# Kernel tuning notes

Hardware: AMD Instinct MI355X
Metric: run time of the kernel (lower is better)

The kernel has to match this reference:

```python
import jax, jax.numpy as jnp
import numpy as np

EPS = 1e-6

def _conv1x1(x, w, bias):
    # x: [b,cin,h,w], w: [cout,cin]
    y = jnp.einsum('bchw,oc->bohw', x, w)
    return y + bias[None, :, None, None]

def _maxpool2(x):
    b, c, h, w = x.shape
    return x.reshape(b, c, h // 2, 2, w // 2, 2).max(axis=(3, 5))

def _up2_align_corners(x):
    # bilinear upsample x2, align_corners=True (matches torch nn.Upsample)
    b, c, h, w = x.shape
    oh, ow = 2 * h, 2 * w
    ys = jnp.linspace(0.0, h - 1.0, oh)
    xs = jnp.linspace(0.0, w - 1.0, ow)
    y0 = jnp.floor(ys).astype(jnp.int32); y1 = jnp.minimum(y0 + 1, h - 1)
    x0 = jnp.floor(xs).astype(jnp.int32); x1 = jnp.minimum(x0 + 1, w - 1)
    ty = (ys - y0).reshape(1, 1, oh, 1)
    tx = (xs - x0).reshape(1, 1, 1, ow)
    r0 = x[:, :, y0, :]; r1 = x[:, :, y1, :]           # [b,c,oh,w]
    v00 = r0[:, :, :, x0]; v01 = r0[:, :, :, x1]       # [b,c,oh,ow]
    v10 = r1[:, :, :, x0]; v11 = r1[:, :, :, x1]
    return (1 - ty) * ((1 - tx) * v00 + tx * v01) + ty * ((1 - tx) * v10 + tx * v11)

def _norm_corr(fm):
    # fm: [b,N,N], indexed [b,p,q]; ReLU then L2-normalize over q for each p
    m = jnp.maximum(fm, 0.0)
    norm = jnp.sqrt(jnp.sum(m * m, axis=2, keepdims=True) + EPS)
    return m / norm

def setup_inputs() -> dict:
    key = jax.random.key(0)
    ks = jax.random.split(key, 8)
    d = {
        'xa': jax.random.normal(ks[0], (8, 256, 64, 64), jnp.float32),
        'xb': jax.random.normal(ks[1], (8, 256, 64, 64), jnp.float32),
        'conv_w': jax.random.normal(ks[2], (1024, 256), jnp.float32) * 0.02,
        'conv_b': jax.random.normal(ks[3], (1024,), jnp.float32) * 0.02,
        'We': jax.random.normal(ks[4], (1024, 1024), jnp.float32) * 0.02,
        'We2': jax.random.normal(ks[5], (1024, 1024), jnp.float32) * 0.02,
        'conv2_w': jax.random.normal(ks[6], (256, 1024), jnp.float32) * 0.02,
        'conv2_b': jax.random.normal(ks[7], (256,), jnp.float32) * 0.02,
    }
    return d

def reference(xa, xb, conv_w, conv_b, We, We2, conv2_w, conv2_b):
    fa = _maxpool2(_conv1x1(xa, conv_w, conv_b))   # [b,c,h,w]
    fb = _maxpool2(_conv1x1(xb, conv_w, conv_b))
    b, c, h, w = fa.shape
    N = h * w
    Fa = fa.reshape(b, c, N)                        # [b,c,N]
    Fb = fb.reshape(b, c, N)
    Fb_t = jnp.swapaxes(Fb, 1, 2)                   # [b,N,c]
    Fa_t = jnp.swapaxes(Fa, 1, 2)
    # fm[b,p,q] = (linear_e(Fb_t) @ Fa)
    fm = jnp.einsum('bpc,cd,bdq->bpq', Fb_t, We.T, Fa)
    Mab = _norm_corr(fm)                            # normalized over q per p
    fm2 = jnp.einsum('bpc,cd,bdq->bpq', Fa_t, We2.T, Fb)
    Mba = _norm_corr(fm2)
    # torch: bmm(corr.view(b,N,N), feat) with corr_flat[b,q,p] = Mn[b,p,q]
    en_a = jnp.einsum('bpq,bpk->bqk', Mab, Fa_t)    # [b,N,c]
    en_b = jnp.einsum('bpq,bpk->bqk', Mba, Fb_t)
    # faithful reinterpretation (torch .view(b,c,h,w) on a [b,N,c] tensor)
    en_a = en_a.reshape(b, c, h, w)
    en_b = en_b.reshape(b, c, h, w)
    en_a = _conv1x1(_up2_align_corners(en_a), conv2_w, conv2_b)
    en_b = _conv1x1(_up2_align_corners(en_b), conv2_w, conv2_b)
    return (en_a, en_b)
```

## Files before the change

### kernel.cpp

```cpp
#include <hip/hip_runtime.h>

typedef unsigned short u16;
typedef short bfrag __attribute__((ext_vector_type(8)));
typedef float facc  __attribute__((ext_vector_type(4)));

__device__ __forceinline__ float bf2f(u16 u) {
    union { unsigned int i; float f; } v; v.i = ((unsigned int)u) << 16; return v.f;
}
__device__ __forceinline__ u16 f2bf(float f) {
    union { float f; unsigned int i; } v; v.f = f;
    unsigned int r = v.i + 0x7FFFu + ((v.i >> 16) & 1u);
    return (u16)(r >> 16);
}

__device__ __forceinline__ u16 ld_bf(const float* p) { return f2bf(*p); }
__device__ __forceinline__ u16 ld_bf(const u16* p)   { return *p; }

__device__ __forceinline__ void store_out(u16* p, float v)   { *p = f2bf(v); }
__device__ __forceinline__ void store_out(float* p, float v) { *p = v; }

__device__ __forceinline__ void gl2lds16(const u16* g, char* l) {
    __builtin_amdgcn_global_load_lds(
        (const __attribute__((address_space(1))) unsigned int*)g,
        (__attribute__((address_space(3))) unsigned int*)l,
        16, 0, 0);
}

__global__ void cvt4_k(const float* __restrict__ s0, u16* __restrict__ d0,
                       const float* __restrict__ s1, u16* __restrict__ d1,
                       const float* __restrict__ s2, u16* __restrict__ d2,
                       const float* __restrict__ s3, u16* __restrict__ d3) {
    int i = blockIdx.x * blockDim.x + threadIdx.x;
    if (i < 262144)        d0[i] = f2bf(s0[i]);
    else if (i < 1310720)  d1[i - 262144] = f2bf(s1[i - 262144]);
    else if (i < 2359296)  d2[i - 1310720] = f2bf(s2[i - 1310720]);
    else                   d3[i - 2359296] = f2bf(s3[i - 2359296]);
}

__global__ void transpose_in_k(const float* __restrict__ srcA,
                               const float* __restrict__ srcB,
                               u16* __restrict__ dst) {
    __shared__ u16 tile[64][65];
    const long SX = 1048576;
    const int z  = blockIdx.z;
    const int c0 = blockIdx.x * 64;
    const int r0 = blockIdx.y * 64;
    const int x  = threadIdx.x;
    const int y0 = threadIdx.y;
    const float* s = (z < 8 ? srcA : srcB) + (size_t)(z & 7) * SX;
    for (int i = 0; i < 8; ++i) {
        int r = y0 + i * 8;
        tile[r][x] = f2bf(s[(size_t)(r0 + r) * 4096 + c0 + x]);
    }
    __syncthreads();
    u16* d = dst + (size_t)z * SX;
    for (int i = 0; i < 8; ++i) {
        int c = y0 + i * 8;
        d[(size_t)(c0 + c) * 256 + r0 + x] = tile[x][c];
    }
}

__global__ void transpose_k(const u16* __restrict__ src, u16* __restrict__ dst,
                            int R, int C, long sStride, long dStride) {
    __shared__ u16 tile[64][65];
    const int b  = blockIdx.z;
    const int c0 = blockIdx.x * 64;
    const int r0 = blockIdx.y * 64;
    const int x  = threadIdx.x;
    const int y0 = threadIdx.y;
    const u16* s = src + (size_t)b * sStride;
    for (int i = 0; i < 8; ++i) {
        int r = y0 + i * 8;
        tile[r][x] = s[(size_t)(r0 + r) * C + c0 + x];
    }
    __syncthreads();
    u16* d = dst + (size_t)b * dStride;
    for (int i = 0; i < 8; ++i) {
        int c = y0 + i * 8;
        d[(size_t)(c0 + c) * R + r0 + x] = tile[x][c];
    }
}

template <typename OutT, int MODE, bool PAIRED>
__global__ __launch_bounds__(256)
void gemm_nt(const u16* __restrict__ A0, const u16* __restrict__ A1, long strideA,
             const u16* __restrict__ B0, const u16* __restrict__ B1, long strideBT,
             OutT* __restrict__ C, long strideC, u16* __restrict__ CT,
             const float* __restrict__ bias, int M, int N, int K) {
    constexpr bool HAS_BIAS = (MODE >= 1);
    constexpr bool POOL     = (MODE == 2);
    constexpr int  SMEM_SZ  = POOL ? 33792 : 16384;
    __shared__ __align__(16) char smem[SMEM_SZ];
    char* AsB = smem;
    char* BsB = smem + 8192;

    const int gx = gridDim.x, gy = gridDim.y;
    long id = blockIdx.x + (long)gx * (blockIdx.y + (long)gy * blockIdx.z);
    long total = (long)gx * gy * gridDim.z;
    long nid = (id & 7) * (total >> 3) + (id >> 3);
    const int bx = (int)(nid % gx);
    long rr = nid / gx;
    const int by = (int)(rr % gy);
    const int b  = (int)(rr / gy);

    const int m0 = bx * 128;
    const int n0 = by * 128;

    const u16* Ab; const u16* Bb;
    if (PAIRED) {
        const int bl = b & 7;
        Ab = (b < 8 ? A0 : A1) + (size_t)bl * strideA;
        Bb = (b < 8 ? B0 : B1) + (size_t)bl * strideBT;
    } else {
        Ab = A0 + (size_t)b * strideA;
        Bb = B0 + (size_t)b * strideBT;
    }

    const int t    = threadIdx.x;
    const int lane = t & 63;
    const int w    = t >> 6;
    const int wm   = (w & 1) * 64;
    const int wn   = (w >> 1) * 64;
    const int q    = lane >> 4;
    const int ln   = lane & 15;

    const int s0 = w * 128 + lane;
    const int s1 = s0 + 64;
    const int r0s = s0 >> 2, c0s = (s0 & 3) * 8;
    const int r1s = s1 >> 2, c1s = (s1 & 3) * 8;

    facc acc[4][4];
    for (int i = 0; i < 4; ++i)
        for (int j = 0; j < 4; ++j)
            acc[i][j] = (facc)0.0f;

    const int nK = K >> 5;
    for (int kt = 0; kt < nK; ++kt) {
        const int k0 = kt << 5;
        gl2lds16(Ab + (size_t)(m0 + r0s) * K + (k0 + c0s), AsB + s0 * 16);
        gl2lds16(Ab + (size_t)(m0 + r1s) * K + (k0 + c1s), AsB + s1 * 16);
        gl2lds16(Bb + (size_t)(n0 + r0s) * K + (k0 + c0s), BsB + s0 * 16);
        gl2lds16(Bb + (size_t)(n0 + r1s) * K + (k0 + c1s), BsB + s1 * 16);
        __syncthreads();
        bfrag af[4], bfr[4];
        for (int mt = 0; mt < 4; ++mt)
            af[mt] = *reinterpret_cast<const bfrag*>(AsB + (wm + mt * 16 + ln) * 64 + q * 16);
        for (int nt = 0; nt < 4; ++nt)
            bfr[nt] = *reinterpret_cast<const bfrag*>(BsB + (wn + nt * 16 + ln) * 64 + q * 16);
        for (int mt = 0; mt < 4; ++mt)
            for (int nt = 0; nt < 4; ++nt)
                acc[mt][nt] = __builtin_amdgcn_mfma_f32_16x16x32_bf16(af[mt], bfr[nt], acc[mt][nt], 0, 0, 0);
        __syncthreads();
    }

    OutT* Cb = C + (size_t)b * strideC;

    if (POOL) {
        float* pool0 = (float*)smem;
        float* pool1 = (float*)(smem + 16896);
        float* pb = (w >> 1) ? pool1 : pool0;
        for (int mt = 0; mt < 4; ++mt) {
            for (int nt = 0; nt < 4; ++nt) {
                for (int r = 0; r < 4; ++r) {
                    int ch = wm + mt * 16 + q * 4 + r;
                    float v = acc[mt][nt][r] + bias[m0 + ch];
                    float vm = fmaxf(v, __shfl_xor(v, 1, 64));
                    if (!(ln & 1))
                        pb[ch * 33 + ((nt * 16 + ln) >> 1)] = vm;
                }
            }
        }
        __syncthreads();
        u16* Cp = (u16*)Cb;
        for (int i = 0; i < 8; ++i) {
            int idx = t + i * 256;
            int ch = idx >> 4, xpp = (idx & 15) * 2;
            float v0 = fmaxf(pool0[ch * 33 + xpp],     pool1[ch * 33 + xpp]);
            float v1 = fmaxf(pool0[ch * 33 + xpp + 1], pool1[ch * 33 + xpp + 1]);
            unsigned pk = (unsigned)f2bf(v0) | ((unsigned)f2bf(v1) << 16);
            *reinterpret_cast<unsigned*>(&Cp[(size_t)(m0 + ch) * 1024 + by * 32 + xpp]) = pk;
            pool0[ch * 33 + xpp] = v0; pool0[ch * 33 + xpp + 1] = v1;
        }
        __syncthreads();
        u16* CTb = CT + (size_t)b * strideC;
        for (int i = 0; i < 8; ++i) {
            int idx = t + i * 256;
            int ch2 = (idx & 63) * 2, xp = idx >> 6;
            unsigned pk = (unsigned)f2bf(pool0[ch2 * 33 + xp]) |
                          ((unsigned)f2bf(pool0[(ch2 + 1) * 33 + xp]) << 16);
            *reinterpret_cast<unsigned*>(&CTb[(size_t)(by * 32 + xp) * 1024 + m0 + ch2]) = pk;
        }
    } else {
        for (int mt = 0; mt < 4; ++mt) {
            const int rbase = m0 + wm + mt * 16 + q * 4;
            for (int nt = 0; nt < 4; ++nt) {
                const int col = n0 + wn + nt * 16 + ln;
                for (int r = 0; r < 4; ++r) {
                    float v = acc[mt][nt][r];
                    if (HAS_BIAS) v += bias[rbase + r];
                    store_out(&Cb[(size_t)(rbase + r) * N + col], v);
                }
            }
        }
    }
}

__global__ void norm_k(const u16* __restrict__ fm, u16* __restrict__ Mout) {
    __shared__ float red[4];
    const long row = blockIdx.x;
    const u16* p = fm + row * 1024;
    const int t = threadIdx.x;
    uint2 raw = *reinterpret_cast<const uint2*>(p + t * 4);
    float v0 = fmaxf(bf2f((u16)(raw.x & 0xFFFF)), 0.f);
    float v1 = fmaxf(bf2f((u16)(raw.x >> 16)), 0.f);
    float v2 = fmaxf(bf2f((u16)(raw.y & 0xFFFF)), 0.f);
    float v3 = fmaxf(bf2f((u16)(raw.y >> 16)), 0.f);
    float s = v0 * v0 + v1 * v1 + v2 * v2 + v3 * v3;
    for (int off = 32; off; off >>= 1) s += __shfl_down(s, off, 64);
    if ((t & 63) == 0) red[t >> 6] = s;
    __syncthreads();
    float total = red[0] + red[1] + red[2] + red[3];
    float inv = 1.0f / sqrtf(total + 1e-6f);
    uint2 o;
    o.x = (unsigned)f2bf(v0 * inv) | ((unsigned)f2bf(v1 * inv) << 16);
    o.y = (unsigned)f2bf(v2 * inv) | ((unsigned)f2bf(v3 * inv) << 16);
    *reinterpret_cast<uint2*>(Mout + row * 1024 + t * 4) = o;
}

__global__ void upsample_k(const float* __restrict__ V, float* __restrict__ out, int total) {
    int idx = blockIdx.x * blockDim.x + threadIdx.x;
    if (idx >= total) return;
    int X  = idx & 63;
    int Y  = (idx >> 6) & 63;
    long bo = idx >> 12;
    const float* p = V + bo * 1024;
    const float sc = 31.0f / 63.0f;
    float ys = Y * sc;
    float xs = X * sc;
    int y0 = (int)ys; int x0 = (int)xs;
    int y1 = y0 + 1; if (y1 > 31) y1 = 31;
    int x1 = x0 + 1; if (x1 > 31) x1 = 31;
    float ty = ys - y0, tx = xs - x0;
    float v00 = p[y0 * 32 + x0], v01 = p[y0 * 32 + x1];
    float v10 = p[y1 * 32 + x0], v11 = p[y1 * 32 + x1];
    out[idx] = (1.f - ty) * ((1.f - tx) * v00 + tx * v01) + ty * ((1.f - tx) * v10 + tx * v11);
}

extern "C" void kernel_launch(void* const* d_in, const int* in_sizes, int n_in,
                              void* d_out, int out_size, void* d_ws, size_t ws_size,
                              hipStream_t stream) {
    const float* xa      = (const float*)d_in[0];
    const float* xb      = (const float*)d_in[1];
    const float* conv_w  = (const float*)d_in[2];
    const float* conv_b  = (const float*)d_in[3];
    const float* We      = (const float*)d_in[4];
    const float* We2     = (const float*)d_in[5];
    const float* conv2_w = (const float*)d_in[6];
    const float* conv2_b = (const float*)d_in[7];
    float* out = (float*)d_out;
    char* ws = (char*)d_ws;

    const long S1M = 1048576;
    const long MiB = 1048576;

    u16*   XT  = (u16*)(ws + 0);
    u16*   T1  = (u16*)(ws + 0);
    u16*   Mb  = (u16*)(ws + 0);
    u16*   Z   = (u16*)(ws + 0);
    u16*   FA  = (u16*)(ws + 32 * MiB);
    u16*   FB  = (u16*)(ws + 48 * MiB);
    u16*   FAT = (u16*)(ws + 64 * MiB);
    u16*   FBT = (u16*)(ws + 80 * MiB);
    float* V   = (float*)(ws + 64 * MiB);
    u16*   FM  = (u16*)(ws + 96 * MiB);
    u16*   MT  = (u16*)(ws + 96 * MiB);
    u16*   CW  = (u16*)(ws + 128 * MiB);
    u16*   WE  = (u16*)(ws + 128 * MiB + 524288);
    u16*   WE2 = (u16*)(ws + 128 * MiB + 2621440);
    u16*   C2W = (u16*)(ws + 128 * MiB + 4718592);

    const dim3 tb64(64, 8);

    cvt4_k<<<10240, 256, 0, stream>>>(conv_w, CW, We, WE, We2, WE2, conv2_w, C2W);

    transpose_in_k<<<dim3(64, 4, 16), tb64, 0, stream>>>(xa, xb, XT);

    gemm_nt<u16, 2, false><<<dim3(8, 32, 16), 256, 0, stream>>>(
        CW, CW, 0, XT, XT, S1M, FA, S1M, FAT, conv_b, 1024, 4096, 256);

    gemm_nt<u16, 0, true><<<dim3(8, 8, 16), 256, 0, stream>>>(
        FBT, FAT, S1M, WE, WE2, 0, T1, S1M, nullptr, nullptr, 1024, 1024, 1024);

    gemm_nt<u16, 0, true><<<dim3(8, 8, 16), 256, 0, stream>>>(
        T1, T1 + 8 * S1M, S1M, FAT, FBT, S1M, FM, S1M, nullptr, nullptr, 1024, 1024, 1024);

    norm_k<<<16384, 256, 0, stream>>>(FM, Mb);

    transpose_k<<<dim3(16, 16, 16), tb64, 0, stream>>>(Mb, MT, 1024, 1024, S1M, S1M);

    gemm_nt<u16, 0, true><<<dim3(8, 8, 16), 256, 0, stream>>>(
        FA, FB, S1M, MT, MT + 8 * S1M, S1M, Z, S1M, nullptr, nullptr, 1024, 1024, 1024);

    gemm_nt<float, 1, false><<<dim3(2, 8, 16), 256, 0, stream>>>(
        C2W, C2W, 0, Z, Z, S1M, V, 256L * 1024, nullptr, conv2_b, 256, 1024, 1024);

    upsample_k<<<65536, 256, 0, stream>>>(V, out, 16 * 256 * 4096);
}
```

Baseline: 461.3 us.

## Deepen GEMM K-tile, stage bf16 epilogue through LDS, fuse norm into transpose

The GEMM now loads a 64-wide K slice per iteration into two 32-wide LDS halves, which halves the number of barrier pairs per tile at the cost of 32 KB of LDS per block. The bf16 output path writes the accumulators into LDS and then stores full 16-byte rows, replacing scattered 2-byte stores. The normalization kernel now only computes per-row inverse norms, and the transpose applies ReLU and scaling while transposing, which removes one full write and read of the normalized matrix. Buffers are remapped in the workspace to fit this new flow.

Result: faster. 421.3 us (-8.7%).

```diff
diff --git a/kernel.cpp b/kernel.cpp
--- a/kernel.cpp
+++ b/kernel.cpp
@@ -12,9 +12,6 @@
     unsigned int r = v.i + 0x7FFFu + ((v.i >> 16) & 1u);
     return (u16)(r >> 16);
 }
-
-__device__ __forceinline__ u16 ld_bf(const float* p) { return f2bf(*p); }
-__device__ __forceinline__ u16 ld_bf(const u16* p)   { return *p; }
 
 __device__ __forceinline__ void store_out(u16* p, float v)   { *p = f2bf(v); }
 __device__ __forceinline__ void store_out(float* p, float v) { *p = v; }
@@ -60,39 +57,17 @@
     }
 }
 
-__global__ void transpose_k(const u16* __restrict__ src, u16* __restrict__ dst,
-                            int R, int C, long sStride, long dStride) {
-    __shared__ u16 tile[64][65];
-    const int b  = blockIdx.z;
-    const int c0 = blockIdx.x * 64;
-    const int r0 = blockIdx.y * 64;
-    const int x  = threadIdx.x;
-    const int y0 = threadIdx.y;
-    const u16* s = src + (size_t)b * sStride;
-    for (int i = 0; i < 8; ++i) {
-        int r = y0 + i * 8;
-        tile[r][x] = s[(size_t)(r0 + r) * C + c0 + x];
-    }
-    __syncthreads();
-    u16* d = dst + (size_t)b * dStride;
-    for (int i = 0; i < 8; ++i) {
-        int c = y0 + i * 8;
-        d[(size_t)(c0 + c) * R + r0 + x] = tile[x][c];
-    }
-}
-
 template <typename OutT, int MODE, bool PAIRED>
 __global__ __launch_bounds__(256)
 void gemm_nt(const u16* __restrict__ A0, const u16* __restrict__ A1, long strideA,
              const u16* __restrict__ B0, const u16* __restrict__ B1, long strideBT,
              OutT* __restrict__ C, long strideC, u16* __restrict__ CT,
              const float* __restrict__ bias, int M, int N, int K) {
-    constexpr bool HAS_BIAS = (MODE >= 1);
-    constexpr bool POOL     = (MODE == 2);
-    constexpr int  SMEM_SZ  = POOL ? 33792 : 16384;
+    constexpr bool POOL    = (MODE == 2);
+    constexpr int  SMEM_SZ = POOL ? 33792 : 32768;
     __shared__ __align__(16) char smem[SMEM_SZ];
-    char* AsB = smem;
-    char* BsB = smem + 8192;
+    char* As = smem;
+    char* Bs = smem + 16384;
 
     const int gx = gridDim.x, gy = gridDim.y;
     long id = blockIdx.x + (long)gx * (blockIdx.y + (long)gy * blockIdx.z);
@@ -124,38 +99,50 @@
     const int q    = lane >> 4;
     const int ln   = lane & 15;
 
-    const int s0 = w * 128 + lane;
-    const int s1 = s0 + 64;
+    const int s0 = w * 64 + lane;
+    const int s1 = s0 + 256;
     const int r0s = s0 >> 2, c0s = (s0 & 3) * 8;
     const int r1s = s1 >> 2, c1s = (s1 & 3) * 8;
+
+    const u16* pA0 = Ab + (size_t)(m0 + r0s) * K + c0s;
+    const u16* pA1 = Ab + (size_t)(m0 + r1s) * K + c1s;
+    const u16* pB0 = Bb + (size_t)(n0 + r0s) * K + c0s;
+    const u16* pB1 = Bb + (size_t)(n0 + r1s) * K + c1s;
 
     facc acc[4][4];
     for (int i = 0; i < 4; ++i)
         for (int j = 0; j < 4; ++j)
             acc[i][j] = (facc)0.0f;
 
-    const int nK = K >> 5;
+    const int nK = K >> 6;
     for (int kt = 0; kt < nK; ++kt) {
-        const int k0 = kt << 5;
-        gl2lds16(Ab + (size_t)(m0 + r0s) * K + (k0 + c0s), AsB + s0 * 16);
-        gl2lds16(Ab + (size_t)(m0 + r1s) * K + (k0 + c1s), AsB + s1 * 16);
-        gl2lds16(Bb + (size_t)(n0 + r0s) * K + (k0 + c0s), BsB + s0 * 16);
-        gl2lds16(Bb + (size_t)(n0 + r1s) * K + (k0 + c1s), BsB + s1 * 16);
-        __syncthreads();
-        bfrag af[4], bfr[4];
-        for (int mt = 0; mt < 4; ++mt)
-            af[mt] = *reinterpret_cast<const bfrag*>(AsB + (wm + mt * 16 + ln) * 64 + q * 16);
-        for (int nt = 0; nt < 4; ++nt)
-            bfr[nt] = *reinterpret_cast<const bfrag*>(BsB + (wn + nt * 16 + ln) * 64 + q * 16);
-        for (int mt = 0; mt < 4; ++mt)
+        const int k0 = kt << 6;
+        gl2lds16(pA0 + k0,      As + s0 * 16);
+        gl2lds16(pA1 + k0,      As + s1 * 16);
+        gl2lds16(pA0 + k0 + 32, As + 8192 + s0 * 16);
+        gl2lds16(pA1 + k0 + 32, As + 8192 + s1 * 16);
+        gl2lds16(pB0 + k0,      Bs + s0 * 16);
+        gl2lds16(pB1 + k0,      Bs + s1 * 16);
+        gl2lds16(pB0 + k0 + 32, Bs + 8192 + s0 * 16);
+        gl2lds16(pB1 + k0 + 32, Bs + 8192 + s1 * 16);
+        __syncthreads();
+        for (int j = 0; j < 2; ++j) {
+            const char* Aj = As + j * 8192;
+            const char* Bj = Bs + j * 8192;
+            bfrag af[4], bfr[4];
+            for (int mt = 0; mt < 4; ++mt)
+                af[mt] = *reinterpret_cast<const bfrag*>(Aj + (wm + mt * 16 + ln) * 64 + q * 16);
             for (int nt = 0; nt < 4; ++nt)
-                acc[mt][nt] = __builtin_amdgcn_mfma_f32_16x16x32_bf16(af[mt], bfr[nt], acc[mt][nt], 0, 0, 0);
-        __syncthreads();
-    }
-
-    OutT* Cb = C + (size_t)b * strideC;
+                bfr[nt] = *reinterpret_cast<const bfrag*>(Bj + (wn + nt * 16 + ln) * 64 + q * 16);
+            for (int mt = 0; mt < 4; ++mt)
+                for (int nt = 0; nt < 4; ++nt)
+                    acc[mt][nt] = __builtin_amdgcn_mfma_f32_16x16x32_bf16(af[mt], bfr[nt], acc[mt][nt], 0, 0, 0);
+        }
+        __syncthreads();
+    }
 
     if (POOL) {
+        u16* Cp  = (u16*)C + (size_t)b * strideC;
         float* pool0 = (float*)smem;
         float* pool1 = (float*)(smem + 16896);
         float* pb = (w >> 1) ? pool1 : pool0;
@@ -171,7 +158,6 @@
             }
         }
         __syncthreads();
-        u16* Cp = (u16*)Cb;
         for (int i = 0; i < 8; ++i) {
             int idx = t + i * 256;
             int ch = idx >> 4, xpp = (idx & 15) * 2;
@@ -190,22 +176,33 @@
                           ((unsigned)f2bf(pool0[(ch2 + 1) * 33 + xp]) << 16);
             *reinterpret_cast<unsigned*>(&CTb[(size_t)(by * 32 + xp) * 1024 + m0 + ch2]) = pk;
         }
+    } else if (MODE == 0) {
+        u16* Cb = (u16*)C + (size_t)b * strideC;
+        u16* dump = (u16*)smem;
+        for (int mt = 0; mt < 4; ++mt)
+            for (int nt = 0; nt < 4; ++nt)
+                for (int r = 0; r < 4; ++r)
+                    dump[(wm + mt * 16 + q * 4 + r) * 128 + wn + nt * 16 + ln] = f2bf(acc[mt][nt][r]);
+        __syncthreads();
+        for (int i = 0; i < 8; ++i) {
+            const int row = w * 32 + i * 4 + (lane >> 4);
+            const uint4 v = *reinterpret_cast<const uint4*>(dump + row * 128 + (lane & 15) * 8);
+            *reinterpret_cast<uint4*>(Cb + (size_t)(m0 + row) * N + n0 + (lane & 15) * 8) = v;
+        }
     } else {
+        OutT* Cb = C + (size_t)b * strideC;
         for (int mt = 0; mt < 4; ++mt) {
             const int rbase = m0 + wm + mt * 16 + q * 4;
             for (int nt = 0; nt < 4; ++nt) {
                 const int col = n0 + wn + nt * 16 + ln;
-                for (int r = 0; r < 4; ++r) {
-                    float v = acc[mt][nt][r];
-                    if (HAS_BIAS) v += bias[rbase + r];
-                    store_out(&Cb[(size_t)(rbase + r) * N + col], v);
-                }
+                for (int r = 0; r < 4; ++r)
+                    store_out(&Cb[(size_t)(rbase + r) * N + col], acc[mt][nt][r] + bias[rbase + r]);
             }
         }
     }
 }
 
-__global__ void norm_k(const u16* __restrict__ fm, u16* __restrict__ Mout) {
+__global__ void norm_rk(const u16* __restrict__ fm, float* __restrict__ rinv) {
     __shared__ float red[4];
     const long row = blockIdx.x;
     const u16* p = fm + row * 1024;
@@ -219,12 +216,33 @@
     for (int off = 32; off; off >>= 1) s += __shfl_down(s, off, 64);
     if ((t & 63) == 0) red[t >> 6] = s;
     __syncthreads();
-    float total = red[0] + red[1] + red[2] + red[3];
-    float inv = 1.0f / sqrtf(total + 1e-6f);
-    uint2 o;
-    o.x = (unsigned)f2bf(v0 * inv) | ((unsigned)f2bf(v1 * inv) << 16);
-    o.y = (unsigned)f2bf(v2 * inv) | ((unsigned)f2bf(v3 * inv) << 16);
-    *reinterpret_cast<uint2*>(Mout + row * 1024 + t * 4) = o;
+    if (t == 0)
+        rinv[row] = 1.0f / sqrtf(red[0] + red[1] + red[2] + red[3] + 1e-6f);
+}
+
+__global__ void transpose_scale_k(const u16* __restrict__ src,
+                                  const float* __restrict__ rinv,
+                                  u16* __restrict__ dst) {
+    __shared__ u16 tile[64][65];
+    const long S = 1048576;
+    const int b  = blockIdx.z;
+    const int c0 = blockIdx.x * 64;
+    const int r0 = blockIdx.y * 64;
+    const int x  = threadIdx.x;
+    const int y0 = threadIdx.y;
+    const u16* s = src + (size_t)b * S;
+    const float* rv = rinv + (size_t)b * 1024;
+    for (int i = 0; i < 8; ++i) {
+        int r = y0 + i * 8;
+        float v = fmaxf(bf2f(s[(size_t)(r0 + r) * 1024 + c0 + x]), 0.f) * rv[r0 + r];
+        tile[r][x] = f2bf(v);
+    }
+    __syncthreads();
+    u16* d = dst + (size_t)b * S;
+    for (int i = 0; i < 8; ++i) {
+        int c = y0 + i * 8;
+        d[(size_t)(c0 + c) * 1024 + r0 + x] = tile[x][c];
+    }
 }
 
 __global__ void upsample_k(const float* __restrict__ V, float* __restrict__ out, int total) {
@@ -265,19 +283,19 @@
 
     u16*   XT  = (u16*)(ws + 0);
     u16*   T1  = (u16*)(ws + 0);
-    u16*   Mb  = (u16*)(ws + 0);
-    u16*   Z   = (u16*)(ws + 0);
+    u16*   MT  = (u16*)(ws + 0);
     u16*   FA  = (u16*)(ws + 32 * MiB);
     u16*   FB  = (u16*)(ws + 48 * MiB);
     u16*   FAT = (u16*)(ws + 64 * MiB);
     u16*   FBT = (u16*)(ws + 80 * MiB);
     float* V   = (float*)(ws + 64 * MiB);
     u16*   FM  = (u16*)(ws + 96 * MiB);
-    u16*   MT  = (u16*)(ws + 96 * MiB);
+    u16*   Z   = (u16*)(ws + 96 * MiB);
     u16*   CW  = (u16*)(ws + 128 * MiB);
     u16*   WE  = (u16*)(ws + 128 * MiB + 524288);
     u16*   WE2 = (u16*)(ws + 128 * MiB + 2621440);
     u16*   C2W = (u16*)(ws + 128 * MiB + 4718592);
+    float* RIV = (float*)(ws + 128 * MiB + 5242880);
 
     const dim3 tb64(64, 8);
 
@@ -294,9 +312,9 @@
     gemm_nt<u16, 0, true><<<dim3(8, 8, 16), 256, 0, stream>>>(
         T1, T1 + 8 * S1M, S1M, FAT, FBT, S1M, FM, S1M, nullptr, nullptr, 1024, 1024, 1024);
 
-    norm_k<<<16384, 256, 0, stream>>>(FM, Mb);
-
-    transpose_k<<<dim3(16, 16, 16), tb64, 0, stream>>>(Mb, MT, 1024, 1024, S1M, S1M);
+    norm_rk<<<16384, 256, 0, stream>>>(FM, RIV);
+
+    transpose_scale_k<<<dim3(16, 16, 16), tb64, 0, stream>>>(FM, RIV, MT);
 
     gemm_nt<u16, 0, true><<<dim3(8, 8, 16), 256, 0, stream>>>(
         FA, FB, S1M, MT, MT + 8 * S1M, S1M, Z, S1M, nullptr, nullptr, 1024, 1024, 1024);
```
